# Performance work log

Hardware: AMD Instinct MI355X
Metric: run time of the kernel (lower is better)

The kernel has to match this reference:

```python
import jax, jax.numpy as jnp
import numpy as np

NUM_HEADS = 16
D_MODEL = 1024
D_QKV = 64


def _xavier(key, shape):
    # xavier normal over last two dims (fan_in = D_MODEL, fan_out = D_QKV)
    std = float(np.sqrt(2.0 / (shape[-2] + shape[-1])))
    return jax.random.normal(key, shape, dtype=jnp.float32) * std


def setup_inputs() -> dict:
    key = jax.random.key(0)
    ks = jax.random.split(key, 9)
    B, L = 4, 2048
    q = jax.random.normal(ks[0], (B, L, D_MODEL), dtype=jnp.float32)
    k = jax.random.normal(ks[1], (B, L, D_MODEL), dtype=jnp.float32)
    v = jax.random.normal(ks[2], (B, L, D_MODEL), dtype=jnp.float32)
    mask = jax.random.randint(ks[3], (B, L, L), 0, 2, dtype=jnp.int32)
    Wq = _xavier(ks[4], (NUM_HEADS, D_MODEL, D_QKV))
    Wk = _xavier(ks[5], (NUM_HEADS, D_MODEL, D_QKV))
    Wv = _xavier(ks[6], (NUM_HEADS, D_MODEL, D_QKV))
    lim = float(1.0 / np.sqrt(D_MODEL))
    Wo_w = jax.random.uniform(ks[7], (D_MODEL, D_MODEL), minval=-lim, maxval=lim, dtype=jnp.float32)
    Wo_b = jax.random.uniform(ks[8], (D_MODEL,), minval=-lim, maxval=lim, dtype=jnp.float32)
    return {"q": q, "k": k, "v": v, "mask": mask,
            "Wq": Wq, "Wk": Wk, "Wv": Wv, "Wo_w": Wo_w, "Wo_b": Wo_b}


def reference(q, k, v, mask, Wq, Wk, Wv, Wo_w, Wo_b):
    B, L, _ = q.shape
    query = jnp.einsum('blm,nmd->bnld', q, Wq)   # [B,H,L,Dq]
    key_ = jnp.einsum('blm,nmd->bnld', k, Wk)
    value = jnp.einsum('blm,nmd->bnld', v, Wv)
    scores = jnp.einsum('bnld,bnmd->bnlm', query, key_) / jnp.sqrt(
        jnp.asarray(D_QKV, dtype=query.dtype))          # [B,H,L,L]
    scores = jnp.where(mask[:, None, :, :] == 0, jnp.asarray(-1e9, scores.dtype), scores)
    attn = jax.nn.softmax(scores, axis=-1)
    out = jnp.einsum('bnlm,bnmd->bnld', attn, value)     # [B,H,L,Dq]
    out = out.transpose(0, 2, 1, 3).reshape(B, L, D_MODEL)
    return out @ Wo_w.T + Wo_b
```

## Files before the change

kernel.cpp:

```cpp
#include <hip/hip_runtime.h>
#include <stdint.h>

typedef __bf16 bf16;
typedef __bf16 bf16x8 __attribute__((ext_vector_type(8)));
typedef float  f32x4  __attribute__((ext_vector_type(4)));
typedef uint32_t u32;
typedef uint64_t u64;

#define SCALE_L2E 0.18033688011112042f

__device__ __forceinline__ void gld_lds16(const void* gsrc, void* ldst) {
  __builtin_amdgcn_global_load_lds(
      (const __attribute__((address_space(1))) void*)gsrc,
      (__attribute__((address_space(3))) void*)ldst, 16, 0, 0);
}


__global__ void cvt3(const float* __restrict__ q, const float* __restrict__ k,
                     const float* __restrict__ v, bf16* __restrict__ out) {
  const float* in = (blockIdx.z == 0) ? q : (blockIdx.z == 1) ? k : v;
  bf16* o = out + (size_t)blockIdx.z * 8388608;
  int stride = gridDim.x * blockDim.x;
  for (int i = blockIdx.x * blockDim.x + threadIdx.x; i < 1048576; i += stride) {
    const float4* p = (const float4*)(in + (size_t)i * 8);
    float4 a = p[0], b = p[1];
    bf16x8 vv;
    vv[0]=(bf16)a.x; vv[1]=(bf16)a.y; vv[2]=(bf16)a.z; vv[3]=(bf16)a.w;
    vv[4]=(bf16)b.x; vv[5]=(bf16)b.y; vv[6]=(bf16)b.z; vv[7]=(bf16)b.w;
    *(bf16x8*)(o + (size_t)i * 8) = vv;
  }
}

__global__ void pack_w(const float* __restrict__ Wq, const float* __restrict__ Wk,
                       const float* __restrict__ Wv, const float* __restrict__ Wo,
                       bf16* __restrict__ Wt) {
  int s = blockIdx.z;
  int tid = blockIdx.x * blockDim.x + threadIdx.x;
  int n = tid >> 7, kb = tid & 127;
  const float* W = (s == 0) ? Wq : (s == 1) ? Wk : (s == 2) ? Wv : Wo;
  bf16x8 v;
  if (s < 3) {
#pragma unroll
    for (int j = 0; j < 8; ++j)
      v[j] = (bf16)W[((n >> 6) << 16) + (kb * 8 + j) * 64 + (n & 63)];
  } else {
    const float4* p = (const float4*)&W[n * 1024 + kb * 8];
    float4 a = p[0], b = p[1];
    v[0]=(bf16)a.x; v[1]=(bf16)a.y; v[2]=(bf16)a.z; v[3]=(bf16)a.w;
    v[4]=(bf16)b.x; v[5]=(bf16)b.y; v[6]=(bf16)b.z; v[7]=(bf16)b.w;
  }
  *(bf16x8*)&Wt[(size_t)s * 1048576 + (size_t)n * 1024 + kb * 8] = v;
}

__global__ void pack_mask(const int* __restrict__ mask, u32* __restrict__ mbits, int total) {
  int stride = gridDim.x * blockDim.x;
  for (int idx = blockIdx.x * blockDim.x + threadIdx.x; idx < total; idx += stride) {
    int v = mask[idx];
    u64 bal = __ballot(v != 0);
    if ((threadIdx.x & 63) == 0)
      *(u64*)&mbits[idx >> 5] = bal;
  }
}

template<int EPI>
__global__ __launch_bounds__(256, 2)
void gemm_bt(const bf16* __restrict__ A, const bf16* __restrict__ Bt,
             void* __restrict__ Cout, void* __restrict__ Cout2,
             const float* __restrict__ bias,
             size_t a_bstride, size_t b_bstride, float cscale) {
  const int gx = gridDim.x;
  int lin = blockIdx.y * gx + blockIdx.x;
  int nwg = gx * gridDim.y;
  int swz = (lin & 7) * (nwg >> 3) + (lin >> 3);
  int bx = swz % gx, by = swz / gx;
  const int bz = blockIdx.z;
  A  += a_bstride * bz;
  Bt += b_bstride * bz;
  const int row0 = by * 128, col0 = bx * 128;
  bool isK = false;
  if (EPI == 0 && row0 >= 8192) { isK = true; Bt += 1048576; }

  __shared__ bf16 sA[2][8192];
  __shared__ bf16 sB[2][8192];

  const int lane = threadIdx.x & 63, w = threadIdx.x >> 6;
  const int c = lane & 15, g = lane >> 4;
  const int wr = w >> 1, wc = w & 1;
  const int c7 = c & 7;

  const int ric = lane >> 3;
  const int pblk = (lane & 7) ^ (ric & 7);
  const bf16* Ap = A + (size_t)row0 * 1024;
  const bf16* Bp = Bt + (size_t)col0 * 1024;
  const bf16* Asrc[4];
  const bf16* Bsrc[4];
#pragma unroll
  for (int ii = 0; ii < 4; ++ii) {
    int r = 8 * (w * 4 + ii) + ric;
    Asrc[ii] = Ap + (size_t)r * 1024 + pblk * 8;
    Bsrc[ii] = Bp + (size_t)r * 1024 + pblk * 8;
  }

  const int y0 = (g ^ c7) << 4;
  const int y1 = ((4 + g) ^ c7) << 4;
  const int abase = wr * 8192 + c * 128;
  const int bbase = wc * 8192 + c * 128;

  f32x4 acc[4][4] = {};

#pragma unroll
  for (int ii = 0; ii < 4; ++ii) {
    gld_lds16(Asrc[ii], (char*)&sA[0][0] + (w * 4 + ii) * 1024);
    gld_lds16(Bsrc[ii], (char*)&sB[0][0] + (w * 4 + ii) * 1024);
  }

  for (int k0 = 0; k0 < 1024; k0 += 64) {
    __syncthreads();
    int cb = (k0 >> 6) & 1, nb = cb ^ 1;
    if (k0 < 960) {
#pragma unroll
      for (int ii = 0; ii < 4; ++ii) {
        gld_lds16(Asrc[ii] + k0 + 64, (char*)&sA[nb][0] + (w * 4 + ii) * 1024);
        gld_lds16(Bsrc[ii] + k0 + 64, (char*)&sB[nb][0] + (w * 4 + ii) * 1024);
      }
    }
    const char* a8 = (const char*)&sA[cb][0] + abase;
    const char* b8 = (const char*)&sB[cb][0] + bbase;
#pragma unroll
    for (int kk = 0; kk < 2; ++kk) {
      const int yk = kk ? y1 : y0;
      bf16x8 af[4], bfr[4];
#pragma unroll
      for (int m = 0; m < 4; ++m)
        af[m] = *(const bf16x8*)(a8 + m * 2048 + yk);
#pragma unroll
      for (int n = 0; n < 4; ++n)
        bfr[n] = *(const bf16x8*)(b8 + n * 2048 + yk);
#pragma unroll
      for (int m = 0; m < 4; ++m)
#pragma unroll
        for (int n = 0; n < 4; ++n)
          acc[m][n] = __builtin_amdgcn_mfma_f32_16x16x32_bf16(af[m], bfr[n], acc[m][n], 0, 0, 0);
    }
  }

  float csc = (EPI == 0 && isK) ? 1.0f : cscale;
#pragma unroll
  for (int m = 0; m < 4; ++m) {
    int row_base = row0 + wr * 64 + m * 16 + g * 4;
#pragma unroll
    for (int n = 0; n < 4; ++n) {
      int col = col0 + wc * 64 + n * 16 + c;
#pragma unroll
      for (int r = 0; r < 4; ++r) {
        int row = row_base + r;
        float val = acc[m][n][r];
        if (EPI == 0) {
          int rl = row & 8191;
          int b = rl >> 11, l = rl & 2047, h = col >> 6, d = col & 63;
          bf16* dst = isK ? (bf16*)Cout2 : (bf16*)Cout;
          dst[(((size_t)(b * 16 + h) * 2048 + l) << 6) + d] = (bf16)(val * csc);
        } else if (EPI == 1) {
          ((bf16*)Cout)[((size_t)(bz * 1024 + row)) * 2048 + col] = (bf16)val;
        } else {
          ((float*)Cout)[(size_t)row * 1024 + col] = val + bias[col];
        }
      }
    }
  }
}

__global__ __launch_bounds__(256, 3)
void attn_fwd(const bf16* __restrict__ Qp, const bf16* __restrict__ Kp,
              const bf16* __restrict__ Vt, const u32* __restrict__ mbits,
              bf16* __restrict__ X) {
  int lin = blockIdx.y * 16 + blockIdx.x;
  int swz = (lin & 7) * 128 + (lin >> 3);
  int qt = swz & 15, bh = swz >> 4;
  int b = bh >> 4, h = bh & 15;
  int q0 = qt * 128;

  const int tid = threadIdx.x;
  const int lane = tid & 63, w = tid >> 6;
  const int c = lane & 15, g = lane >> 4;

  __shared__ char smem[49152];
  char* sKV = smem;
  char* sPw = smem + 32768 + w * 4096;

  const int c7 = c & 7;
  const int y0 = (g ^ c7) << 4;
  const int y1 = ((4 + g) ^ c7) << 4;
  const int ko0 = c * 128 + y0;
  const int ko1 = c * 128 + y1;
  const int vo0 = 8192 + c * 128 + y0;
  const int vo1 = 8192 + c * 128 + y1;
  const char* paddr0 = sPw + c * 128 + y0;
  const char* paddr1 = sPw + c * 128 + y1;
  char* pw[4];
#pragma unroll
  for (int nk = 0; nk < 4; ++nk)
    pw[nk] = sPw + c * 128 + ((g & 1) * 8) + (((nk * 2 + (g >> 1)) ^ c7) << 4);

  const int r0 = tid >> 3, bb0 = tid & 7;
  const int r1 = (256 + tid) >> 3, bb1 = tid & 7;
  const int dK0 = r0 * 128 + ((bb0 ^ (r0 & 7)) << 4);
  const int dK1 = r1 * 128 + ((bb1 ^ (r1 & 7)) << 4);
  const int dV0 = 8192 + dK0;
  const int dV1 = 8192 + dK1;
  const bf16* gK0 = Kp + (size_t)bh * 131072 + r0 * 64 + bb0 * 8;
  const bf16* gK1 = Kp + (size_t)bh * 131072 + r1 * 64 + bb1 * 8;
  const bf16* gV0 = Vt + ((size_t)(b * 1024 + h * 64 + r0)) * 2048 + bb0 * 8;
  const bf16* gV1 = Vt + ((size_t)(b * 1024 + h * 64 + r1)) * 2048 + bb1 * 8;

  const bf16* Qbase = Qp + ((size_t)bh * 2048) * 64;
  bf16x8 qf[2][2];
#pragma unroll
  for (int nq = 0; nq < 2; ++nq) {
    int qg = q0 + w * 32 + nq * 16 + c;
#pragma unroll
    for (int kk = 0; kk < 2; ++kk)
      qf[nq][kk] = *(const bf16x8*)&Qbase[(size_t)qg * 64 + kk * 32 + g * 8];
  }

  bf16x8 onesv;
#pragma unroll
  for (int i = 0; i < 8; ++i) onesv[i] = (bf16)1.0f;

  const u64* Mrow0 = (const u64*)(mbits + ((size_t)b * 2048 + (q0 + w * 32 + c)) * 64);
  const u64* Mrow1 = (const u64*)(mbits + ((size_t)b * 2048 + (q0 + w * 32 + 16 + c)) * 64);

  f32x4 oacc[4][2] = {};
  f32x4 dacc[2] = {};

  {
    uint4 kr0 = *(const uint4*)gK0, kr1 = *(const uint4*)gK1;
    uint4 vr0 = *(const uint4*)gV0, vr1 = *(const uint4*)gV1;
    *(uint4*)(sKV + dK0) = kr0; *(uint4*)(sKV + dK1) = kr1;
    *(uint4*)(sKV + dV0) = vr0; *(uint4*)(sKV + dV1) = vr1;
  }
  u64 mw0 = Mrow0[0], mw1 = Mrow1[0];

  for (int t = 0; t < 32; ++t) {
    __syncthreads();
    const char* kbuf = sKV + ((t & 1) << 14);

    uint4 kr0, kr1, vr0, vr1;
    u64 mn0 = 0, mn1 = 0;
    if (t < 31) {
      kr0 = *(const uint4*)(gK0 + (size_t)(t + 1) * 4096);
      kr1 = *(const uint4*)(gK1 + (size_t)(t + 1) * 4096);
      vr0 = *(const uint4*)(gV0 + (size_t)(t + 1) * 64);
      vr1 = *(const uint4*)(gV1 + (size_t)(t + 1) * 64);
      mn0 = Mrow0[t + 1];
      mn1 = Mrow1[t + 1];
    }

    f32x4 st[4][2] = {};
    __builtin_amdgcn_s_setprio(1);
#pragma unroll
    for (int nk = 0; nk < 4; ++nk) {
      bf16x8 kfa = *(const bf16x8*)(kbuf + ko0 + nk * 2048);
      st[nk][0] = __builtin_amdgcn_mfma_f32_16x16x32_bf16(kfa, qf[0][0], st[nk][0], 0, 0, 0);
      st[nk][1] = __builtin_amdgcn_mfma_f32_16x16x32_bf16(kfa, qf[1][0], st[nk][1], 0, 0, 0);
      bf16x8 kfb = *(const bf16x8*)(kbuf + ko1 + nk * 2048);
      st[nk][0] = __builtin_amdgcn_mfma_f32_16x16x32_bf16(kfb, qf[0][1], st[nk][0], 0, 0, 0);
      st[nk][1] = __builtin_amdgcn_mfma_f32_16x16x32_bf16(kfb, qf[1][1], st[nk][1], 0, 0, 0);
    }
    __builtin_amdgcn_s_setprio(0);

#pragma unroll
    for (int nq = 0; nq < 2; ++nq) {
      u64 ms = (nq ? mw1 : mw0) >> (4 * g);
      u32 ma = (u32)ms;
      u32 mb2 = (u32)(ms >> 32);
#pragma unroll
      for (int nk = 0; nk < 4; ++nk) {
        u32 msel = (nk < 2) ? ma : mb2;
        const int bs = (nk & 1) * 16;
        float e0 = __builtin_amdgcn_exp2f(st[nk][nq][0]);
        float e1 = __builtin_amdgcn_exp2f(st[nk][nq][1]);
        float e2 = __builtin_amdgcn_exp2f(st[nk][nq][2]);
        float e3 = __builtin_amdgcn_exp2f(st[nk][nq][3]);
        e0 = (msel & (1u << (bs + 0))) ? e0 : 0.f;
        e1 = (msel & (1u << (bs + 1))) ? e1 : 0.f;
        e2 = (msel & (1u << (bs + 2))) ? e2 : 0.f;
        e3 = (msel & (1u << (bs + 3))) ? e3 : 0.f;
        union { bf16 hh[4]; uint2 dd; } pk;
        pk.hh[0] = (bf16)e0; pk.hh[1] = (bf16)e1;
        pk.hh[2] = (bf16)e2; pk.hh[3] = (bf16)e3;
        *(uint2*)(pw[nk] + nq * 2048) = pk.dd;
      }
    }

    __builtin_amdgcn_s_setprio(1);
#pragma unroll
    for (int kk = 0; kk < 2; ++kk) {
      const char* pa = kk ? paddr1 : paddr0;
      const int vo = kk ? vo1 : vo0;
      bf16x8 pf0 = *(const bf16x8*)(pa);
      bf16x8 pf1 = *(const bf16x8*)(pa + 2048);
      dacc[0] = __builtin_amdgcn_mfma_f32_16x16x32_bf16(onesv, pf0, dacc[0], 0, 0, 0);
      dacc[1] = __builtin_amdgcn_mfma_f32_16x16x32_bf16(onesv, pf1, dacc[1], 0, 0, 0);
#pragma unroll
      for (int md = 0; md < 4; ++md) {
        bf16x8 vf = *(const bf16x8*)(kbuf + vo + md * 2048);
        oacc[md][0] = __builtin_amdgcn_mfma_f32_16x16x32_bf16(vf, pf0, oacc[md][0], 0, 0, 0);
        oacc[md][1] = __builtin_amdgcn_mfma_f32_16x16x32_bf16(vf, pf1, oacc[md][1], 0, 0, 0);
      }
    }
    __builtin_amdgcn_s_setprio(0);

    if (t < 31) {
      char* nbuf = sKV + (((t + 1) & 1) << 14);
      *(uint4*)(nbuf + dK0) = kr0; *(uint4*)(nbuf + dK1) = kr1;
      *(uint4*)(nbuf + dV0) = vr0; *(uint4*)(nbuf + dV1) = vr1;
    }
    mw0 = mn0; mw1 = mn1;
  }

  float inv0 = 1.f / dacc[0][0];
  float inv1 = 1.f / dacc[1][0];

  __syncthreads();
  char* Xl = smem;
#pragma unroll
  for (int nq = 0; nq < 2; ++nq) {
    float inv = nq ? inv1 : inv0;
    int ql = w * 32 + nq * 16 + c;
#pragma unroll
    for (int md = 0; md < 4; ++md)
#pragma unroll
      for (int r = 0; r < 4; ++r) {
        int d = md * 16 + g * 4 + r;
        int blk = d >> 3, off = d & 7;
        *(bf16*)(Xl + ql * 128 + ((blk ^ (ql & 7)) << 4) + off * 2) =
            (bf16)(oacc[md][nq][r] * inv);
      }
  }
  __syncthreads();
#pragma unroll
  for (int i = 0; i < 4; ++i) {
    int u = i * 256 + tid;
    int row = u >> 3, blk = u & 7;
    uint4 xv = *(const uint4*)(Xl + row * 128 + ((blk ^ (row & 7)) << 4));
    *(uint4*)&X[(size_t)(b * 2048 + q0 + row) * 1024 + h * 64 + blk * 8] = xv;
  }
}


extern "C" void kernel_launch(void* const* d_in, const int* in_sizes, int n_in,
                              void* d_out, int out_size, void* d_ws, size_t ws_size,
                              hipStream_t stream) {
  const float* q    = (const float*)d_in[0];
  const float* k    = (const float*)d_in[1];
  const float* v    = (const float*)d_in[2];
  const int*   mask = (const int*)d_in[3];
  const float* Wq   = (const float*)d_in[4];
  const float* Wk   = (const float*)d_in[5];
  const float* Wv   = (const float*)d_in[6];
  const float* Wo   = (const float*)d_in[7];
  const float* Wb   = (const float*)d_in[8];

  char* ws = (char*)d_ws;
  bf16* qb = (bf16*)(ws + 0);
  bf16* kb = (bf16*)(ws + 16777216);
  bf16* vb = (bf16*)(ws + 33554432);
  bf16* Wt = (bf16*)(ws + 50331648);
  bf16* Qp = (bf16*)(ws + 58720256);
  bf16* Kp = (bf16*)(ws + 75497472);
  bf16* Vt = (bf16*)(ws + 92274688);
  bf16* Xb = (bf16*)(ws + 109051904);
  u32*  mb = (u32*) (ws + 125829120);

  cvt3<<<dim3(512, 1, 3), 256, 0, stream>>>(q, k, v, qb);
  pack_w<<<dim3(512, 1, 4), 256, 0, stream>>>(Wq, Wk, Wv, Wo, Wt);
  pack_mask<<<2048, 256, 0, stream>>>(mask, mb, 16777216);

  gemm_bt<0><<<dim3(8, 128, 1), 256, 0, stream>>>(qb, Wt, Qp, Kp, nullptr, 0, 0, SCALE_L2E);
  gemm_bt<1><<<dim3(16, 8, 4), 256, 0, stream>>>(Wt + 2097152, vb, Vt, nullptr, nullptr, 0, 2097152, 1.0f);

  attn_fwd<<<dim3(16, 64, 1), 256, 0, stream>>>(Qp, Kp, Vt, mb, Xb);

  gemm_bt<2><<<dim3(8, 64, 1), 256, 0, stream>>>(Xb, Wt + 3145728, (float*)d_out, nullptr, Wb, 0, 0, 1.0f);
}
```

Measured before the change: 263.6 us.

## Fuse prep kernels, merge Q/K/V projections, shrink attention KV tile

Three preprocessing kernels (input cast, weight pack, mask bit-pack) are merged into one launch, and the Q/K and V projection GEMMs are merged into a single grid. The goal is to cut launch overhead and tail idle time between small kernels. The attention kernel's KV tile is halved from 64 to 32 keys per iteration, which halves shared memory and raises the occupancy hint from 3 to 4 blocks per CU. The cost is twice as many loop iterations and barriers, and more per-iteration overhead in attention.

```diff
diff --git a/kernel.cpp b/kernel.cpp
--- a/kernel.cpp
+++ b/kernel.cpp
@@ -15,136 +15,183 @@
       (__attribute__((address_space(3))) void*)ldst, 16, 0, 0);
 }
 
-
-__global__ void cvt3(const float* __restrict__ q, const float* __restrict__ k,
-                     const float* __restrict__ v, bf16* __restrict__ out) {
-  const float* in = (blockIdx.z == 0) ? q : (blockIdx.z == 1) ? k : v;
-  bf16* o = out + (size_t)blockIdx.z * 8388608;
-  int stride = gridDim.x * blockDim.x;
-  for (int i = blockIdx.x * blockDim.x + threadIdx.x; i < 1048576; i += stride) {
-    const float4* p = (const float4*)(in + (size_t)i * 8);
-    float4 a = p[0], b = p[1];
+__global__ void prep(const float* __restrict__ q, const float* __restrict__ k,
+                     const float* __restrict__ v, const int* __restrict__ mask,
+                     const float* __restrict__ Wq, const float* __restrict__ Wk,
+                     const float* __restrict__ Wv, const float* __restrict__ Wo,
+                     bf16* __restrict__ qkv, bf16* __restrict__ Wt, u32* __restrict__ mbits) {
+  const int z = blockIdx.z;
+  const int tg = blockIdx.x * 256 + threadIdx.x;
+  if (z < 3) {
+    const float* in = (z == 0) ? q : (z == 1) ? k : v;
+    bf16* o = qkv + (size_t)z * 8388608;
+#pragma unroll
+    for (int it = 0; it < 2; ++it) {
+      int i = tg + it * 524288;
+      const float4* p = (const float4*)(in + (size_t)i * 8);
+      float4 a = p[0], b = p[1];
+      bf16x8 vv;
+      vv[0]=(bf16)a.x; vv[1]=(bf16)a.y; vv[2]=(bf16)a.z; vv[3]=(bf16)a.w;
+      vv[4]=(bf16)b.x; vv[5]=(bf16)b.y; vv[6]=(bf16)b.z; vv[7]=(bf16)b.w;
+      *(bf16x8*)(o + (size_t)i * 8) = vv;
+    }
+  } else if (z == 3) {
+    int s = tg >> 17;
+    int t = tg & 131071;
+    int n = t >> 7, kb = t & 127;
+    const float* W = (s == 0) ? Wq : (s == 1) ? Wk : (s == 2) ? Wv : Wo;
     bf16x8 vv;
-    vv[0]=(bf16)a.x; vv[1]=(bf16)a.y; vv[2]=(bf16)a.z; vv[3]=(bf16)a.w;
-    vv[4]=(bf16)b.x; vv[5]=(bf16)b.y; vv[6]=(bf16)b.z; vv[7]=(bf16)b.w;
-    *(bf16x8*)(o + (size_t)i * 8) = vv;
-  }
-}
-
-__global__ void pack_w(const float* __restrict__ Wq, const float* __restrict__ Wk,
-                       const float* __restrict__ Wv, const float* __restrict__ Wo,
-                       bf16* __restrict__ Wt) {
-  int s = blockIdx.z;
-  int tid = blockIdx.x * blockDim.x + threadIdx.x;
-  int n = tid >> 7, kb = tid & 127;
-  const float* W = (s == 0) ? Wq : (s == 1) ? Wk : (s == 2) ? Wv : Wo;
-  bf16x8 v;
-  if (s < 3) {
-#pragma unroll
-    for (int j = 0; j < 8; ++j)
-      v[j] = (bf16)W[((n >> 6) << 16) + (kb * 8 + j) * 64 + (n & 63)];
+    if (s < 3) {
+#pragma unroll
+      for (int j = 0; j < 8; ++j)
+        vv[j] = (bf16)W[((n >> 6) << 16) + (kb * 8 + j) * 64 + (n & 63)];
+    } else {
+      const float4* p = (const float4*)&W[n * 1024 + kb * 8];
+      float4 a = p[0], b = p[1];
+      vv[0]=(bf16)a.x; vv[1]=(bf16)a.y; vv[2]=(bf16)a.z; vv[3]=(bf16)a.w;
+      vv[4]=(bf16)b.x; vv[5]=(bf16)b.y; vv[6]=(bf16)b.z; vv[7]=(bf16)b.w;
+    }
+    *(bf16x8*)&Wt[(size_t)s * 1048576 + (size_t)n * 1024 + kb * 8] = vv;
   } else {
-    const float4* p = (const float4*)&W[n * 1024 + kb * 8];
-    float4 a = p[0], b = p[1];
-    v[0]=(bf16)a.x; v[1]=(bf16)a.y; v[2]=(bf16)a.z; v[3]=(bf16)a.w;
-    v[4]=(bf16)b.x; v[5]=(bf16)b.y; v[6]=(bf16)b.z; v[7]=(bf16)b.w;
-  }
-  *(bf16x8*)&Wt[(size_t)s * 1048576 + (size_t)n * 1024 + kb * 8] = v;
-}
-
-__global__ void pack_mask(const int* __restrict__ mask, u32* __restrict__ mbits, int total) {
-  int stride = gridDim.x * blockDim.x;
-  for (int idx = blockIdx.x * blockDim.x + threadIdx.x; idx < total; idx += stride) {
-    int v = mask[idx];
-    u64 bal = __ballot(v != 0);
-    if ((threadIdx.x & 63) == 0)
-      *(u64*)&mbits[idx >> 5] = bal;
-  }
-}
-
-template<int EPI>
+    for (int idx = tg; idx < 16777216; idx += 524288) {
+      int m = mask[idx];
+      u64 bal = __ballot(m != 0);
+      if ((threadIdx.x & 63) == 0)
+        *(u64*)&mbits[idx >> 5] = bal;
+    }
+  }
+}
+
+
+#define GEMM_CORE(Ap_, Bp_)                                                    \
+  __shared__ bf16 sA[2][8192];                                                 \
+  __shared__ bf16 sB[2][8192];                                                 \
+  const int lane = threadIdx.x & 63, w = threadIdx.x >> 6;                     \
+  const int c = lane & 15, g = lane >> 4;                                      \
+  const int wr = w >> 1, wc = w & 1;                                           \
+  const int c7 = c & 7;                                                        \
+  const int ric = lane >> 3;                                                   \
+  const int pblk = (lane & 7) ^ (ric & 7);                                     \
+  const bf16* Asrc[4];                                                         \
+  const bf16* Bsrc[4];                                                         \
+  _Pragma("unroll")                                                            \
+  for (int ii = 0; ii < 4; ++ii) {                                             \
+    int r = 8 * (w * 4 + ii) + ric;                                            \
+    Asrc[ii] = (Ap_) + (size_t)r * 1024 + pblk * 8;                            \
+    Bsrc[ii] = (Bp_) + (size_t)r * 1024 + pblk * 8;                            \
+  }                                                                            \
+  const int y0 = (g ^ c7) << 4;                                                \
+  const int y1 = ((4 + g) ^ c7) << 4;                                          \
+  const int abase = wr * 8192 + c * 128;                                       \
+  const int bbase = wc * 8192 + c * 128;                                       \
+  f32x4 acc[4][4] = {};                                                        \
+  _Pragma("unroll")                                                            \
+  for (int ii = 0; ii < 4; ++ii) {                                             \
+    gld_lds16(Asrc[ii], (char*)&sA[0][0] + (w * 4 + ii) * 1024);               \
+    gld_lds16(Bsrc[ii], (char*)&sB[0][0] + (w * 4 + ii) * 1024);               \
+  }                                                                            \
+  for (int k0 = 0; k0 < 1024; k0 += 64) {                                      \
+    __syncthreads();                                                           \
+    int cb = (k0 >> 6) & 1, nb = cb ^ 1;                                       \
+    if (k0 < 960) {                                                            \
+      _Pragma("unroll")                                                        \
+      for (int ii = 0; ii < 4; ++ii) {                                         \
+        gld_lds16(Asrc[ii] + k0 + 64, (char*)&sA[nb][0] + (w * 4 + ii) * 1024);\
+        gld_lds16(Bsrc[ii] + k0 + 64, (char*)&sB[nb][0] + (w * 4 + ii) * 1024);\
+      }                                                                        \
+    }                                                                          \
+    const char* a8 = (const char*)&sA[cb][0] + abase;                          \
+    const char* b8 = (const char*)&sB[cb][0] + bbase;                          \
+    _Pragma("unroll")                                                          \
+    for (int kk = 0; kk < 2; ++kk) {                                           \
+      const int yk = kk ? y1 : y0;                                             \
+      bf16x8 af[4], bfr[4];                                                    \
+      _Pragma("unroll")                                                        \
+      for (int m = 0; m < 4; ++m)                                              \
+        af[m] = *(const bf16x8*)(a8 + m * 2048 + yk);                          \
+      _Pragma("unroll")                                                        \
+      for (int n = 0; n < 4; ++n)                                              \
+        bfr[n] = *(const bf16x8*)(b8 + n * 2048 + yk);                         \
+      _Pragma("unroll")                                                        \
+      for (int m = 0; m < 4; ++m)                                              \
+        _Pragma("unroll")                                                      \
+        for (int n = 0; n < 4; ++n)                                            \
+          acc[m][n] = __builtin_amdgcn_mfma_f32_16x16x32_bf16(af[m], bfr[n], acc[m][n], 0, 0, 0); \
+    }                                                                          \
+  }
+
 __global__ __launch_bounds__(256, 2)
-void gemm_bt(const bf16* __restrict__ A, const bf16* __restrict__ Bt,
-             void* __restrict__ Cout, void* __restrict__ Cout2,
-             const float* __restrict__ bias,
-             size_t a_bstride, size_t b_bstride, float cscale) {
-  const int gx = gridDim.x;
-  int lin = blockIdx.y * gx + blockIdx.x;
-  int nwg = gx * gridDim.y;
-  int swz = (lin & 7) * (nwg >> 3) + (lin >> 3);
-  int bx = swz % gx, by = swz / gx;
-  const int bz = blockIdx.z;
-  A  += a_bstride * bz;
-  Bt += b_bstride * bz;
+void proj_fused(const bf16* __restrict__ qkv, const bf16* __restrict__ Wt,
+                bf16* __restrict__ Qp, bf16* __restrict__ Kp, bf16* __restrict__ Vt) {
+  const int wg = blockIdx.x;
+  const bf16* Ap;
+  const bf16* Bp;
+  int row0, col0, stage;
+  if (wg < 1024) {
+    int swz = (wg & 7) * 128 + (wg >> 3);
+    int bx = swz & 7, by = swz >> 3;
+    row0 = by * 128; col0 = bx * 128;
+    stage = (row0 >= 8192) ? 1 : 0;
+    Ap = qkv + (size_t)row0 * 1024;
+    Bp = Wt + (stage ? 1048576 : 0) + (size_t)col0 * 1024;
+  } else {
+    int w2 = wg - 1024;
+    int bz = w2 >> 7, rem = w2 & 127;
+    int swz = (rem & 7) * 16 + (rem >> 3);
+    int bx = swz & 15, by = swz >> 4;
+    row0 = by * 128; col0 = bx * 128;
+    stage = 2 + bz;
+    Ap = Wt + 2097152 + (size_t)row0 * 1024;
+    Bp = qkv + 16777216 + (size_t)bz * 2097152 + (size_t)col0 * 1024;
+  }
+
+  GEMM_CORE(Ap, Bp)
+
+  if (stage <= 1) {
+    float csc = stage ? 1.0f : SCALE_L2E;
+    bf16* dst = stage ? Kp : Qp;
+#pragma unroll
+    for (int m = 0; m < 4; ++m) {
+      int row_base = (row0 & 8191) + wr * 64 + m * 16 + g * 4;
+#pragma unroll
+      for (int n = 0; n < 4; ++n) {
+        int col = col0 + wc * 64 + n * 16 + c;
+#pragma unroll
+        for (int r = 0; r < 4; ++r) {
+          int row = row_base + r;
+          int b = row >> 11, l = row & 2047, h = col >> 6, d = col & 63;
+          dst[(((size_t)(b * 16 + h) * 2048 + l) << 6) + d] = (bf16)(acc[m][n][r] * csc);
+        }
+      }
+    }
+  } else {
+    int bz = stage - 2;
+#pragma unroll
+    for (int m = 0; m < 4; ++m) {
+      int row_base = row0 + wr * 64 + m * 16 + g * 4;
+#pragma unroll
+      for (int n = 0; n < 4; ++n) {
+        int col = col0 + wc * 64 + n * 16 + c;
+#pragma unroll
+        for (int r = 0; r < 4; ++r)
+          Vt[((size_t)(bz * 1024 + row_base + r)) * 2048 + col] = (bf16)acc[m][n][r];
+      }
+    }
+  }
+}
+
+__global__ __launch_bounds__(256, 2)
+void gemm_out(const bf16* __restrict__ X, const bf16* __restrict__ Wot,
+              float* __restrict__ out, const float* __restrict__ bias) {
+  int lin = blockIdx.y * 8 + blockIdx.x;
+  int swz = (lin & 7) * 64 + (lin >> 3);
+  int bx = swz & 7, by = swz >> 3;
   const int row0 = by * 128, col0 = bx * 128;
-  bool isK = false;
-  if (EPI == 0 && row0 >= 8192) { isK = true; Bt += 1048576; }
-
-  __shared__ bf16 sA[2][8192];
-  __shared__ bf16 sB[2][8192];
-
-  const int lane = threadIdx.x & 63, w = threadIdx.x >> 6;
-  const int c = lane & 15, g = lane >> 4;
-  const int wr = w >> 1, wc = w & 1;
-  const int c7 = c & 7;
-
-  const int ric = lane >> 3;
-  const int pblk = (lane & 7) ^ (ric & 7);
-  const bf16* Ap = A + (size_t)row0 * 1024;
-  const bf16* Bp = Bt + (size_t)col0 * 1024;
-  const bf16* Asrc[4];
-  const bf16* Bsrc[4];
-#pragma unroll
-  for (int ii = 0; ii < 4; ++ii) {
-    int r = 8 * (w * 4 + ii) + ric;
-    Asrc[ii] = Ap + (size_t)r * 1024 + pblk * 8;
-    Bsrc[ii] = Bp + (size_t)r * 1024 + pblk * 8;
-  }
-
-  const int y0 = (g ^ c7) << 4;
-  const int y1 = ((4 + g) ^ c7) << 4;
-  const int abase = wr * 8192 + c * 128;
-  const int bbase = wc * 8192 + c * 128;
-
-  f32x4 acc[4][4] = {};
-
-#pragma unroll
-  for (int ii = 0; ii < 4; ++ii) {
-    gld_lds16(Asrc[ii], (char*)&sA[0][0] + (w * 4 + ii) * 1024);
-    gld_lds16(Bsrc[ii], (char*)&sB[0][0] + (w * 4 + ii) * 1024);
-  }
-
-  for (int k0 = 0; k0 < 1024; k0 += 64) {
-    __syncthreads();
-    int cb = (k0 >> 6) & 1, nb = cb ^ 1;
-    if (k0 < 960) {
-#pragma unroll
-      for (int ii = 0; ii < 4; ++ii) {
-        gld_lds16(Asrc[ii] + k0 + 64, (char*)&sA[nb][0] + (w * 4 + ii) * 1024);
-        gld_lds16(Bsrc[ii] + k0 + 64, (char*)&sB[nb][0] + (w * 4 + ii) * 1024);
-      }
-    }
-    const char* a8 = (const char*)&sA[cb][0] + abase;
-    const char* b8 = (const char*)&sB[cb][0] + bbase;
-#pragma unroll
-    for (int kk = 0; kk < 2; ++kk) {
-      const int yk = kk ? y1 : y0;
-      bf16x8 af[4], bfr[4];
-#pragma unroll
-      for (int m = 0; m < 4; ++m)
-        af[m] = *(const bf16x8*)(a8 + m * 2048 + yk);
-#pragma unroll
-      for (int n = 0; n < 4; ++n)
-        bfr[n] = *(const bf16x8*)(b8 + n * 2048 + yk);
-#pragma unroll
-      for (int m = 0; m < 4; ++m)
-#pragma unroll
-        for (int n = 0; n < 4; ++n)
-          acc[m][n] = __builtin_amdgcn_mfma_f32_16x16x32_bf16(af[m], bfr[n], acc[m][n], 0, 0, 0);
-    }
-  }
-
-  float csc = (EPI == 0 && isK) ? 1.0f : cscale;
+  const bf16* Ap = X + (size_t)row0 * 1024;
+  const bf16* Bp = Wot + (size_t)col0 * 1024;
+
+  GEMM_CORE(Ap, Bp)
+
 #pragma unroll
   for (int m = 0; m < 4; ++m) {
     int row_base = row0 + wr * 64 + m * 16 + g * 4;
@@ -152,25 +199,13 @@
     for (int n = 0; n < 4; ++n) {
       int col = col0 + wc * 64 + n * 16 + c;
 #pragma unroll
-      for (int r = 0; r < 4; ++r) {
-        int row = row_base + r;
-        float val = acc[m][n][r];
-        if (EPI == 0) {
-          int rl = row & 8191;
-          int b = rl >> 11, l = rl & 2047, h = col >> 6, d = col & 63;
-          bf16* dst = isK ? (bf16*)Cout2 : (bf16*)Cout;
-          dst[(((size_t)(b * 16 + h) * 2048 + l) << 6) + d] = (bf16)(val * csc);
-        } else if (EPI == 1) {
-          ((bf16*)Cout)[((size_t)(bz * 1024 + row)) * 2048 + col] = (bf16)val;
-        } else {
-          ((float*)Cout)[(size_t)row * 1024 + col] = val + bias[col];
-        }
-      }
-    }
-  }
-}
-
-__global__ __launch_bounds__(256, 3)
+      for (int r = 0; r < 4; ++r)
+        out[(size_t)(row_base + r) * 1024 + col] = acc[m][n][r] + bias[col];
+    }
+  }
+}
+
+__global__ __launch_bounds__(256, 4)
 void attn_fwd(const bf16* __restrict__ Qp, const bf16* __restrict__ Kp,
               const bf16* __restrict__ Vt, const u32* __restrict__ mbits,
               bf16* __restrict__ X) {
@@ -184,34 +219,25 @@
   const int lane = tid & 63, w = tid >> 6;
   const int c = lane & 15, g = lane >> 4;
 
-  __shared__ char smem[49152];
+  __shared__ char smem[24576];
   char* sKV = smem;
-  char* sPw = smem + 32768 + w * 4096;
+  char* sPw = smem + 16384 + w * 2048;
 
   const int c7 = c & 7;
-  const int y0 = (g ^ c7) << 4;
-  const int y1 = ((4 + g) ^ c7) << 4;
-  const int ko0 = c * 128 + y0;
-  const int ko1 = c * 128 + y1;
-  const int vo0 = 8192 + c * 128 + y0;
-  const int vo1 = 8192 + c * 128 + y1;
-  const char* paddr0 = sPw + c * 128 + y0;
-  const char* paddr1 = sPw + c * 128 + y1;
-  char* pw[4];
-#pragma unroll
-  for (int nk = 0; nk < 4; ++nk)
-    pw[nk] = sPw + c * 128 + ((g & 1) * 8) + (((nk * 2 + (g >> 1)) ^ c7) << 4);
-
-  const int r0 = tid >> 3, bb0 = tid & 7;
-  const int r1 = (256 + tid) >> 3, bb1 = tid & 7;
-  const int dK0 = r0 * 128 + ((bb0 ^ (r0 & 7)) << 4);
-  const int dK1 = r1 * 128 + ((bb1 ^ (r1 & 7)) << 4);
-  const int dV0 = 8192 + dK0;
-  const int dV1 = 8192 + dK1;
-  const bf16* gK0 = Kp + (size_t)bh * 131072 + r0 * 64 + bb0 * 8;
-  const bf16* gK1 = Kp + (size_t)bh * 131072 + r1 * 64 + bb1 * 8;
-  const bf16* gV0 = Vt + ((size_t)(b * 1024 + h * 64 + r0)) * 2048 + bb0 * 8;
-  const bf16* gV1 = Vt + ((size_t)(b * 1024 + h * 64 + r1)) * 2048 + bb1 * 8;
+  const int ko0 = c * 128 + ((g ^ c7) << 4);
+  const int ko1 = c * 128 + (((4 + g) ^ c7) << 4);
+  const int pr_off = (c >> 1) * 128 + ((((c & 1) * 4 + g) ^ (c >> 1)) << 4);
+  int pwo[2];
+#pragma unroll
+  for (int nk = 0; nk < 2; ++nk)
+    pwo[nk] = (c >> 1) * 128 + ((((c & 1) * 4 + nk * 2 + (g >> 1)) ^ (c >> 1)) << 4) + (g & 1) * 8;
+
+  const int kr_ = tid >> 3, kb_ = tid & 7;
+  const int dK = kr_ * 128 + ((kb_ ^ (kr_ & 7)) << 4);
+  const int vd_ = tid >> 2, vk_ = tid & 3;
+  const int dV = 4096 + (vd_ >> 1) * 128 + (((((vd_ & 1) << 2) + vk_) ^ ((vd_ >> 1) & 7)) << 4);
+  const bf16* gK = Kp + (size_t)bh * 131072 + kr_ * 64 + kb_ * 8;
+  const bf16* gV = Vt + ((size_t)(b * 1024 + h * 64 + vd_)) * 2048 + vk_ * 8;
 
   const bf16* Qbase = Qp + ((size_t)bh * 2048) * 64;
   bf16x8 qf[2][2];
@@ -227,39 +253,37 @@
 #pragma unroll
   for (int i = 0; i < 8; ++i) onesv[i] = (bf16)1.0f;
 
-  const u64* Mrow0 = (const u64*)(mbits + ((size_t)b * 2048 + (q0 + w * 32 + c)) * 64);
-  const u64* Mrow1 = (const u64*)(mbits + ((size_t)b * 2048 + (q0 + w * 32 + 16 + c)) * 64);
+  const u32* Mrow0 = mbits + ((size_t)b * 2048 + (q0 + w * 32 + c)) * 64;
+  const u32* Mrow1 = mbits + ((size_t)b * 2048 + (q0 + w * 32 + 16 + c)) * 64;
 
   f32x4 oacc[4][2] = {};
   f32x4 dacc[2] = {};
 
   {
-    uint4 kr0 = *(const uint4*)gK0, kr1 = *(const uint4*)gK1;
-    uint4 vr0 = *(const uint4*)gV0, vr1 = *(const uint4*)gV1;
-    *(uint4*)(sKV + dK0) = kr0; *(uint4*)(sKV + dK1) = kr1;
-    *(uint4*)(sKV + dV0) = vr0; *(uint4*)(sKV + dV1) = vr1;
-  }
-  u64 mw0 = Mrow0[0], mw1 = Mrow1[0];
-
-  for (int t = 0; t < 32; ++t) {
+    uint4 kr = *(const uint4*)gK;
+    uint4 vr = *(const uint4*)gV;
+    *(uint4*)(sKV + dK) = kr;
+    *(uint4*)(sKV + dV) = vr;
+  }
+  u32 mw0 = Mrow0[0], mw1 = Mrow1[0];
+
+  for (int t = 0; t < 64; ++t) {
     __syncthreads();
-    const char* kbuf = sKV + ((t & 1) << 14);
-
-    uint4 kr0, kr1, vr0, vr1;
-    u64 mn0 = 0, mn1 = 0;
-    if (t < 31) {
-      kr0 = *(const uint4*)(gK0 + (size_t)(t + 1) * 4096);
-      kr1 = *(const uint4*)(gK1 + (size_t)(t + 1) * 4096);
-      vr0 = *(const uint4*)(gV0 + (size_t)(t + 1) * 64);
-      vr1 = *(const uint4*)(gV1 + (size_t)(t + 1) * 64);
+    const char* kbuf = sKV + ((t & 1) << 13);
+
+    uint4 kr, vr;
+    u32 mn0 = 0, mn1 = 0;
+    if (t < 63) {
+      kr = *(const uint4*)(gK + (size_t)(t + 1) * 2048);
+      vr = *(const uint4*)(gV + (size_t)(t + 1) * 32);
       mn0 = Mrow0[t + 1];
       mn1 = Mrow1[t + 1];
     }
 
-    f32x4 st[4][2] = {};
+    f32x4 st[2][2] = {};
     __builtin_amdgcn_s_setprio(1);
 #pragma unroll
-    for (int nk = 0; nk < 4; ++nk) {
+    for (int nk = 0; nk < 2; ++nk) {
       bf16x8 kfa = *(const bf16x8*)(kbuf + ko0 + nk * 2048);
       st[nk][0] = __builtin_amdgcn_mfma_f32_16x16x32_bf16(kfa, qf[0][0], st[nk][0], 0, 0, 0);
       st[nk][1] = __builtin_amdgcn_mfma_f32_16x16x32_bf16(kfa, qf[1][0], st[nk][1], 0, 0, 0);
@@ -271,50 +295,44 @@
 
 #pragma unroll
     for (int nq = 0; nq < 2; ++nq) {
-      u64 ms = (nq ? mw1 : mw0) >> (4 * g);
-      u32 ma = (u32)ms;
-      u32 mb2 = (u32)(ms >> 32);
-#pragma unroll
-      for (int nk = 0; nk < 4; ++nk) {
-        u32 msel = (nk < 2) ? ma : mb2;
-        const int bs = (nk & 1) * 16;
+      u32 ms = (nq ? mw1 : mw0) >> (4 * g);
+#pragma unroll
+      for (int nk = 0; nk < 2; ++nk) {
+        const int bs = nk * 16;
         float e0 = __builtin_amdgcn_exp2f(st[nk][nq][0]);
         float e1 = __builtin_amdgcn_exp2f(st[nk][nq][1]);
         float e2 = __builtin_amdgcn_exp2f(st[nk][nq][2]);
         float e3 = __builtin_amdgcn_exp2f(st[nk][nq][3]);
-        e0 = (msel & (1u << (bs + 0))) ? e0 : 0.f;
-        e1 = (msel & (1u << (bs + 1))) ? e1 : 0.f;
-        e2 = (msel & (1u << (bs + 2))) ? e2 : 0.f;
-        e3 = (msel & (1u << (bs + 3))) ? e3 : 0.f;
+        e0 = (ms & (1u << (bs + 0))) ? e0 : 0.f;
+        e1 = (ms & (1u << (bs + 1))) ? e1 : 0.f;
+        e2 = (ms & (1u << (bs + 2))) ? e2 : 0.f;
+        e3 = (ms & (1u << (bs + 3))) ? e3 : 0.f;
         union { bf16 hh[4]; uint2 dd; } pk;
         pk.hh[0] = (bf16)e0; pk.hh[1] = (bf16)e1;
         pk.hh[2] = (bf16)e2; pk.hh[3] = (bf16)e3;
-        *(uint2*)(pw[nk] + nq * 2048) = pk.dd;
+        *(uint2*)(sPw + pwo[nk] + nq * 1024) = pk.dd;
       }
     }
 
     __builtin_amdgcn_s_setprio(1);
-#pragma unroll
-    for (int kk = 0; kk < 2; ++kk) {
-      const char* pa = kk ? paddr1 : paddr0;
-      const int vo = kk ? vo1 : vo0;
-      bf16x8 pf0 = *(const bf16x8*)(pa);
-      bf16x8 pf1 = *(const bf16x8*)(pa + 2048);
+    {
+      bf16x8 pf0 = *(const bf16x8*)(sPw + pr_off);
+      bf16x8 pf1 = *(const bf16x8*)(sPw + pr_off + 1024);
       dacc[0] = __builtin_amdgcn_mfma_f32_16x16x32_bf16(onesv, pf0, dacc[0], 0, 0, 0);
       dacc[1] = __builtin_amdgcn_mfma_f32_16x16x32_bf16(onesv, pf1, dacc[1], 0, 0, 0);
 #pragma unroll
       for (int md = 0; md < 4; ++md) {
-        bf16x8 vf = *(const bf16x8*)(kbuf + vo + md * 2048);
+        bf16x8 vf = *(const bf16x8*)(kbuf + 4096 + pr_off + md * 1024);
         oacc[md][0] = __builtin_amdgcn_mfma_f32_16x16x32_bf16(vf, pf0, oacc[md][0], 0, 0, 0);
         oacc[md][1] = __builtin_amdgcn_mfma_f32_16x16x32_bf16(vf, pf1, oacc[md][1], 0, 0, 0);
       }
     }
     __builtin_amdgcn_s_setprio(0);
 
-    if (t < 31) {
-      char* nbuf = sKV + (((t + 1) & 1) << 14);
-      *(uint4*)(nbuf + dK0) = kr0; *(uint4*)(nbuf + dK1) = kr1;
-      *(uint4*)(nbuf + dV0) = vr0; *(uint4*)(nbuf + dV1) = vr1;
+    if (t < 63) {
+      char* nbuf = sKV + (((t + 1) & 1) << 13);
+      *(uint4*)(nbuf + dK) = kr;
+      *(uint4*)(nbuf + dV) = vr;
     }
     mw0 = mn0; mw1 = mn1;
   }
@@ -363,24 +381,19 @@
   const float* Wb   = (const float*)d_in[8];
 
   char* ws = (char*)d_ws;
-  bf16* qb = (bf16*)(ws + 0);
-  bf16* kb = (bf16*)(ws + 16777216);
-  bf16* vb = (bf16*)(ws + 33554432);
-  bf16* Wt = (bf16*)(ws + 50331648);
-  bf16* Qp = (bf16*)(ws + 58720256);
-  bf16* Kp = (bf16*)(ws + 75497472);
-  bf16* Vt = (bf16*)(ws + 92274688);
-  bf16* Xb = (bf16*)(ws + 109051904);
-  u32*  mb = (u32*) (ws + 125829120);
-
-  cvt3<<<dim3(512, 1, 3), 256, 0, stream>>>(q, k, v, qb);
-  pack_w<<<dim3(512, 1, 4), 256, 0, stream>>>(Wq, Wk, Wv, Wo, Wt);
-  pack_mask<<<2048, 256, 0, stream>>>(mask, mb, 16777216);
-
-  gemm_bt<0><<<dim3(8, 128, 1), 256, 0, stream>>>(qb, Wt, Qp, Kp, nullptr, 0, 0, SCALE_L2E);
-  gemm_bt<1><<<dim3(16, 8, 4), 256, 0, stream>>>(Wt + 2097152, vb, Vt, nullptr, nullptr, 0, 2097152, 1.0f);
+  bf16* qkv = (bf16*)(ws + 0);
+  bf16* Wt  = (bf16*)(ws + 50331648);
+  bf16* Qp  = (bf16*)(ws + 58720256);
+  bf16* Kp  = (bf16*)(ws + 75497472);
+  bf16* Vt  = (bf16*)(ws + 92274688);
+  bf16* Xb  = (bf16*)(ws + 109051904);
+  u32*  mb  = (u32*) (ws + 125829120);
+
+  prep<<<dim3(2048, 1, 5), 256, 0, stream>>>(q, k, v, mask, Wq, Wk, Wv, Wo, qkv, Wt, mb);
+
+  proj_fused<<<dim3(1536, 1, 1), 256, 0, stream>>>(qkv, Wt, Qp, Kp, Vt);
 
   attn_fwd<<<dim3(16, 64, 1), 256, 0, stream>>>(Qp, Kp, Vt, mb, Xb);
 
-  gemm_bt<2><<<dim3(8, 64, 1), 256, 0, stream>>>(Xb, Wt + 3145728, (float*)d_out, nullptr, Wb, 0, 0, 1.0f);
-}
+  gemm_out<<<dim3(8, 64, 1), 256, 0, stream>>>(Xb, Wt + 3145728, (float*)d_out, Wb);
+}
```

Result: no change. 261.5 us (-0.8%).
